# Kernel optimization log

Hardware: AMD Instinct MI355X
Metric: run time of the kernel (lower is better)

## Reference

```python
import jax, jax.numpy as jnp
import numpy as np

T, H, F, E, K, C = 8192, 1024, 2048, 16, 2, 1280  # tokens, hidden, ffn, experts, top_k, capacity


def setup_inputs() -> dict:
    key = jax.random.key(0)
    ks = jax.random.split(key, 6)
    return {
        "x": jax.random.normal(ks[0], (T, H), dtype=jnp.float32),
        "w_router": jax.random.normal(ks[1], (H, E), dtype=jnp.float32) * 0.02,
        "w1": jax.random.normal(ks[2], (E, H, F), dtype=jnp.float32) * 0.02,
        "b1": jnp.zeros((E, F), dtype=jnp.float32),
        "w2": jax.random.normal(ks[3], (E, F, H), dtype=jnp.float32) * 0.02,
        "b2": jnp.zeros((E, H), dtype=jnp.float32),
    }


def reference(x, w_router, w1, b1, w2, b2):
    # ---- Router: softmax + top-k (TopKRouter) ----
    logits = x @ w_router                                  # [T, E]
    probs = jax.nn.softmax(logits, axis=-1)
    topk_p, topk_idx = jax.lax.top_k(probs, K)             # [T, K]
    topk_p = topk_p / jnp.sum(topk_p, axis=-1, keepdims=True)

    # ---- Dispatch with capacity drop (token_permutation) ----
    flat_e = topk_idx.reshape(-1)                          # [T*K] expert id per assignment
    token_ids = jnp.repeat(jnp.arange(T), K)               # [T*K]
    oh = jax.nn.one_hot(flat_e, E, dtype=jnp.int32)        # [T*K, E]
    # position of each assignment within its expert's buffer (token order)
    pos = jnp.cumsum(oh, axis=0) - oh                      # [T*K, E]
    pos = jnp.take_along_axis(pos, flat_e[:, None], axis=1)[:, 0]  # [T*K]
    keep = pos < C
    safe_pos = jnp.where(keep, pos, C)                     # dropped tokens -> dummy slot C

    dispatched = jnp.zeros((E, C + 1, H), dtype=x.dtype)
    dispatched = dispatched.at[flat_e, safe_pos].add(x[token_ids])
    disp = dispatched[:, :C, :]                            # [E, C, H]

    # ---- Grouped expert MLP (SequentialMLP: fc1 -> gelu -> fc2) ----
    h = jax.nn.gelu(jnp.einsum("ech,ehf->ecf", disp, w1) + b1[:, None, :])
    y = jnp.einsum("ecf,efh->ech", h, w2) + b2[:, None, :]  # [E, C, H]

    # ---- Combine (token_unpermutation): gather + prob-weighted sum ----
    y_pad = jnp.pad(y, ((0, 0), (0, 1), (0, 0)))            # dummy slot returns garbage, masked below
    gathered = y_pad[flat_e, safe_pos]                      # [T*K, H]
    gathered = jnp.where(keep[:, None], gathered, 0.0)
    weighted = gathered * topk_p.reshape(-1)[:, None]
    out = jax.ops.segment_sum(weighted, token_ids, num_segments=T)  # [T, H]
    return out
```

## Files before the change

kernel.cpp:

```cpp
#include <hip/hip_runtime.h>
#include <cstdint>
#include <cstddef>

#define T_TOK 8192
#define HDIM  1024
#define FDIM  2048
#define NEXP  16
#define CAP   1280

typedef __bf16 bf16x8 __attribute__((ext_vector_type(8)));
typedef float  f32x4  __attribute__((ext_vector_type(4)));

__device__ inline void gld16(const void* g, void* l) {
  __builtin_amdgcn_global_load_lds(
      (__attribute__((address_space(1))) void*)g,
      (__attribute__((address_space(3))) void*)l, 16, 0, 0);
}

__global__ __launch_bounds__(256) void router_kernel(
    const float* __restrict__ x, const float* __restrict__ wr,
    int* __restrict__ eidx, float* __restrict__ eprob) {
  int t = blockIdx.x * 4 + (threadIdx.x >> 6);
  int lane = threadIdx.x & 63;
  float acc[NEXP];
#pragma unroll
  for (int e = 0; e < NEXP; ++e) acc[e] = 0.f;
  const float4* xp = (const float4*)(x + (size_t)t * HDIM + lane * 16);
#pragma unroll
  for (int q = 0; q < 4; ++q) {
    float4 xv = xp[q];
    float xa[4] = {xv.x, xv.y, xv.z, xv.w};
#pragma unroll
    for (int ii = 0; ii < 4; ++ii) {
      int h = lane * 16 + q * 4 + ii;
      const float4* wp = (const float4*)(wr + (size_t)h * NEXP);
      float w[NEXP];
      float4 w0 = wp[0], w1 = wp[1], w2 = wp[2], w3 = wp[3];
      w[0]=w0.x; w[1]=w0.y; w[2]=w0.z; w[3]=w0.w;
      w[4]=w1.x; w[5]=w1.y; w[6]=w1.z; w[7]=w1.w;
      w[8]=w2.x; w[9]=w2.y; w[10]=w2.z; w[11]=w2.w;
      w[12]=w3.x; w[13]=w3.y; w[14]=w3.z; w[15]=w3.w;
#pragma unroll
      for (int e = 0; e < NEXP; ++e) acc[e] += xa[ii] * w[e];
    }
  }
#pragma unroll
  for (int e = 0; e < NEXP; ++e) {
#pragma unroll
    for (int s = 32; s > 0; s >>= 1) acc[e] += __shfl_xor(acc[e], s);
  }
  if (lane == 0) {
    float l0 = -1e30f, l1 = -1e30f; int i0 = 0, i1 = 0;
#pragma unroll
    for (int e = 0; e < NEXP; ++e) {
      float v = acc[e];
      if (v > l0) { l1 = l0; i1 = i0; l0 = v; i0 = e; }
      else if (v > l1) { l1 = v; i1 = e; }
    }
    float p0 = 1.f / (1.f + __expf(l1 - l0));
    eidx[t * 2 + 0] = i0; eidx[t * 2 + 1] = i1;
    eprob[t * 2 + 0] = p0; eprob[t * 2 + 1] = 1.f - p0;
  }
}

__global__ __launch_bounds__(256) void pos_kernel(
    const int* __restrict__ eidx, const float* __restrict__ eprob,
    int* __restrict__ slot_token, float* __restrict__ slot_prob) {
  __shared__ int scan[256][NEXP];
  int tid = threadIdx.x;
  int cnt[NEXP];
#pragma unroll
  for (int e = 0; e < NEXP; ++e) cnt[e] = 0;
  int base_i = tid * 64;
  for (int i = 0; i < 64; ++i) cnt[eidx[base_i + i]]++;
#pragma unroll
  for (int e = 0; e < NEXP; ++e) scan[tid][e] = cnt[e];
  __syncthreads();
  if (tid < NEXP) {
    int run = 0;
    for (int i = 0; i < 256; ++i) { int v = scan[i][tid]; scan[i][tid] = run; run += v; }
  }
  __syncthreads();
  int basec[NEXP];
#pragma unroll
  for (int e = 0; e < NEXP; ++e) basec[e] = scan[tid][e];
  for (int i = 0; i < 64; ++i) {
    int fi = base_i + i;
    int e = eidx[fi];
    int p = basec[e]++;
    if (p < CAP) {
      slot_token[e * CAP + p] = fi >> 1;
      slot_prob[e * CAP + p] = eprob[fi];
    }
  }
}

__global__ __launch_bounds__(256) void scatter_kernel(
    const float* __restrict__ x, const int* __restrict__ slot_token,
    __bf16* __restrict__ disp) {
  int s = blockIdx.x * 4 + (threadIdx.x >> 6);
  int lane = threadIdx.x & 63;
  int tok = slot_token[s];
  __bf16 vals[16] __attribute__((aligned(16)));
  if (tok >= 0) {
    const float4* xp = (const float4*)(x + (size_t)tok * HDIM + lane * 16);
#pragma unroll
    for (int q = 0; q < 4; ++q) {
      float4 v = xp[q];
      vals[q * 4 + 0] = (__bf16)v.x; vals[q * 4 + 1] = (__bf16)v.y;
      vals[q * 4 + 2] = (__bf16)v.z; vals[q * 4 + 3] = (__bf16)v.w;
    }
  } else {
#pragma unroll
    for (int q = 0; q < 16; ++q) vals[q] = (__bf16)0.f;
  }
  uint4* dst = (uint4*)(disp + (size_t)s * HDIM + lane * 16);
  dst[0] = ((uint4*)vals)[0];
  dst[1] = ((uint4*)vals)[1];
}

__global__ __launch_bounds__(256) void transpose_cast_kernel(
    const float* __restrict__ src, __bf16* __restrict__ dst, int R, int Cc) {
  int e = blockIdx.z;
  src += (size_t)e * R * Cc;
  dst += (size_t)e * R * Cc;
  __shared__ float tile[64][65];
  int gy = blockIdx.y * 64;
  int gx = blockIdx.x * 64;
  int tid = threadIdx.x;
  int r = tid >> 4;
  int c4 = (tid & 15) * 4;
#pragma unroll
  for (int rr = 0; rr < 4; ++rr) {
    float4 v = *(const float4*)(src + (size_t)(gy + r + rr * 16) * Cc + gx + c4);
    tile[r + rr * 16][c4 + 0] = v.x;
    tile[r + rr * 16][c4 + 1] = v.y;
    tile[r + rr * 16][c4 + 2] = v.z;
    tile[r + rr * 16][c4 + 3] = v.w;
  }
  __syncthreads();
  int r2 = tid >> 2;
  int cb = (tid & 3) * 16;
  __bf16 o[16] __attribute__((aligned(16)));
#pragma unroll
  for (int i = 0; i < 16; ++i) o[i] = (__bf16)tile[cb + i][r2];
  uint4* dp = (uint4*)(dst + (size_t)(gx + r2) * R + gy + cb);
  dp[0] = ((uint4*)o)[0];
  dp[1] = ((uint4*)o)[1];
}

template <int EPI>
__global__ __launch_bounds__(256) void moe_gemm_kernel(
    const __bf16* __restrict__ A, const __bf16* __restrict__ Bt,
    const float* __restrict__ bias, __bf16* __restrict__ Hout,
    const int* __restrict__ slot_token, const float* __restrict__ slot_prob,
    float* __restrict__ out, int M, int N, int Kd) {
  const int e = blockIdx.z;
  const int m0 = blockIdx.y * 128, n0 = blockIdx.x * 128;
  const __bf16* Ae = A + (size_t)e * M * Kd;
  const __bf16* Be = Bt + (size_t)e * N * Kd;
  __shared__ __bf16 ldsA[128 * 64];
  __shared__ __bf16 ldsB[128 * 64];
  const int tid = threadIdx.x, wave = tid >> 6, lane = tid & 63;
  const int quad = lane >> 4, l15 = lane & 15;
  const int wm = (wave >> 1) * 64, wn = (wave & 1) * 64;
  f32x4 acc[4][4] = {};
  const int Kb = Kd * 2;
  const int ktiles = Kd >> 6;
  for (int kt = 0; kt < ktiles; ++kt) {
    __syncthreads();
#pragma unroll
    for (int rr = 0; rr < 4; ++rr) {
      int bofs = wave * 4096 + rr * 1024;
      int lofs = bofs + lane * 16;
      int row = lofs >> 7;
      int colb = lofs & 127;
      gld16((const char*)Ae + (size_t)(m0 + row) * Kb + kt * 128 + colb,
            (char*)ldsA + bofs);
      gld16((const char*)Be + (size_t)(n0 + row) * Kb + kt * 128 + colb,
            (char*)ldsB + bofs);
    }
    __syncthreads();
#pragma unroll
    for (int kk = 0; kk < 64; kk += 32) {
      bf16x8 av[4], bv[4];
#pragma unroll
      for (int i = 0; i < 4; ++i)
        av[i] = *(const bf16x8*)&ldsA[(wm + i * 16 + l15) * 64 + kk + quad * 8];
#pragma unroll
      for (int j = 0; j < 4; ++j)
        bv[j] = *(const bf16x8*)&ldsB[(wn + j * 16 + l15) * 64 + kk + quad * 8];
#pragma unroll
      for (int i = 0; i < 4; ++i)
#pragma unroll
        for (int j = 0; j < 4; ++j)
          acc[i][j] = __builtin_amdgcn_mfma_f32_16x16x32_bf16(av[i], bv[j], acc[i][j], 0, 0, 0);
    }
  }
  if (EPI == 1) {
    __bf16* He = Hout + (size_t)e * M * N;
#pragma unroll
    for (int i = 0; i < 4; ++i) {
#pragma unroll
      for (int r = 0; r < 4; ++r) {
        int m = m0 + wm + i * 16 + quad * 4 + r;
#pragma unroll
        for (int j = 0; j < 4; ++j) {
          int n = n0 + wn + j * 16 + l15;
          float v = acc[i][j][r] + bias[(size_t)e * N + n];
          float u = 0.7978845608028654f * (v + 0.044715f * v * v * v);
          float ex = __expf(-2.f * fabsf(u));
          float th = (1.f - ex) / (1.f + ex);
          th = copysignf(th, u);
          He[(size_t)m * N + n] = (__bf16)(0.5f * v * (1.f + th));
        }
      }
    }
  } else {
    const int* st = slot_token + e * CAP;
    const float* sp = slot_prob + e * CAP;
#pragma unroll
    for (int i = 0; i < 4; ++i) {
#pragma unroll
      for (int r = 0; r < 4; ++r) {
        int m = m0 + wm + i * 16 + quad * 4 + r;
        int tok = st[m];
        if (tok >= 0) {
          float p = sp[m];
#pragma unroll
          for (int j = 0; j < 4; ++j) {
            int n = n0 + wn + j * 16 + l15;
            float v = acc[i][j][r] + bias[(size_t)e * N + n];
            atomicAdd(out + (size_t)tok * HDIM + n, p * v);
          }
        }
      }
    }
  }
}

extern "C" void kernel_launch(void* const* d_in, const int* in_sizes, int n_in,
                              void* d_out, int out_size, void* d_ws, size_t ws_size,
                              hipStream_t stream) {
  const float* x  = (const float*)d_in[0];
  const float* wr = (const float*)d_in[1];
  const float* w1 = (const float*)d_in[2];
  const float* b1 = (const float*)d_in[3];
  const float* w2 = (const float*)d_in[4];
  const float* b2 = (const float*)d_in[5];
  float* out = (float*)d_out;

  char* ws = (char*)d_ws;
  size_t off = 0;
  __bf16* w1t = (__bf16*)(ws + off); off += (size_t)NEXP * FDIM * HDIM * 2;
  __bf16* w2t = (__bf16*)(ws + off); off += (size_t)NEXP * HDIM * FDIM * 2;
  __bf16* disp = (__bf16*)(ws + off); off += (size_t)NEXP * CAP * HDIM * 2;
  __bf16* hbuf = (__bf16*)(ws + off); off += (size_t)NEXP * CAP * FDIM * 2;
  int*   slot_token = (int*)(ws + off);  off += (size_t)NEXP * CAP * 4;
  float* slot_prob  = (float*)(ws + off); off += (size_t)NEXP * CAP * 4;
  int*   eidx  = (int*)(ws + off);  off += (size_t)T_TOK * 2 * 4;
  float* eprob = (float*)(ws + off); off += (size_t)T_TOK * 2 * 4;
  if (ws_size < off) return;

  hipMemsetAsync(slot_token, 0xFF, (size_t)NEXP * CAP * 4, stream);
  hipMemsetAsync(d_out, 0, (size_t)T_TOK * HDIM * 4, stream);

  transpose_cast_kernel<<<dim3(FDIM / 64, HDIM / 64, NEXP), 256, 0, stream>>>(w1, w1t, HDIM, FDIM);
  transpose_cast_kernel<<<dim3(HDIM / 64, FDIM / 64, NEXP), 256, 0, stream>>>(w2, w2t, FDIM, HDIM);

  router_kernel<<<T_TOK / 4, 256, 0, stream>>>(x, wr, eidx, eprob);
  pos_kernel<<<1, 256, 0, stream>>>(eidx, eprob, slot_token, slot_prob);
  scatter_kernel<<<NEXP * CAP / 4, 256, 0, stream>>>(x, slot_token, disp);

  moe_gemm_kernel<1><<<dim3(FDIM / 128, CAP / 128, NEXP), 256, 0, stream>>>(
      disp, w1t, b1, hbuf, nullptr, nullptr, nullptr, CAP, FDIM, HDIM);
  moe_gemm_kernel<2><<<dim3(HDIM / 128, CAP / 128, NEXP), 256, 0, stream>>>(
      hbuf, w2t, b2, nullptr, slot_token, slot_prob, out, CAP, HDIM, FDIM);
}
```

Before: 888.0 us.

## Double-buffer MoE GEMM LDS tiles with XOR swizzle and vectorize pos counting

The grouped GEMM now keeps two LDS buffers, so the global-to-LDS load of the next K tile is issued before the MFMA work on the current one, with a single waitcnt+barrier per iteration. The global source columns are XOR-swizzled by row so the LDS reads for MFMA operands avoid bank conflicts. The pos kernel's expert-count loop also reads eidx as int4. LDS use doubles to 64KB per block, which may lower occupancy. Correctness of the single-barrier scheme depends on the vmcnt wait covering the LDS-direct loads.

```diff
diff --git a/kernel.cpp b/kernel.cpp
--- a/kernel.cpp
+++ b/kernel.cpp
@@ -72,7 +72,11 @@
 #pragma unroll
   for (int e = 0; e < NEXP; ++e) cnt[e] = 0;
   int base_i = tid * 64;
-  for (int i = 0; i < 64; ++i) cnt[eidx[base_i + i]]++;
+  const int4* ep = (const int4*)(eidx + base_i);
+  for (int i = 0; i < 16; ++i) {
+    int4 v = ep[i];
+    cnt[v.x]++; cnt[v.y]++; cnt[v.z]++; cnt[v.w]++;
+  }
 #pragma unroll
   for (int e = 0; e < NEXP; ++e) scan[tid][e] = cnt[e];
   __syncthreads();
@@ -159,37 +163,61 @@
   const int m0 = blockIdx.y * 128, n0 = blockIdx.x * 128;
   const __bf16* Ae = A + (size_t)e * M * Kd;
   const __bf16* Be = Bt + (size_t)e * N * Kd;
-  __shared__ __bf16 ldsA[128 * 64];
-  __shared__ __bf16 ldsB[128 * 64];
+  __shared__ __bf16 lds[2 * 2 * 8192];
   const int tid = threadIdx.x, wave = tid >> 6, lane = tid & 63;
   const int quad = lane >> 4, l15 = lane & 15;
   const int wm = (wave >> 1) * 64, wn = (wave & 1) * 64;
   f32x4 acc[4][4] = {};
   const int Kb = Kd * 2;
   const int ktiles = Kd >> 6;
+
+  const int bofs0 = wave * 4096;
+  int srow[4], sgcol[4];
+#pragma unroll
+  for (int rr = 0; rr < 4; ++rr) {
+    int lofs = bofs0 + rr * 1024 + lane * 16;
+    int row = lofs >> 7;
+    int chunk = (lofs >> 4) & 7;
+    srow[rr] = row;
+    sgcol[rr] = (chunk ^ (row & 7)) * 16;
+  }
+
+  auto stage = [&](int kt, int b) {
+    char* dstA = (char*)lds + b * 32768;
+    char* dstB = dstA + 16384;
+#pragma unroll
+    for (int rr = 0; rr < 4; ++rr) {
+      int bofs = bofs0 + rr * 1024;
+      gld16((const char*)Ae + (size_t)(m0 + srow[rr]) * Kb + kt * 128 + sgcol[rr],
+            dstA + bofs);
+      gld16((const char*)Be + (size_t)(n0 + srow[rr]) * Kb + kt * 128 + sgcol[rr],
+            dstB + bofs);
+    }
+  };
+
+  stage(0, 0);
   for (int kt = 0; kt < ktiles; ++kt) {
-    __syncthreads();
-#pragma unroll
-    for (int rr = 0; rr < 4; ++rr) {
-      int bofs = wave * 4096 + rr * 1024;
-      int lofs = bofs + lane * 16;
-      int row = lofs >> 7;
-      int colb = lofs & 127;
-      gld16((const char*)Ae + (size_t)(m0 + row) * Kb + kt * 128 + colb,
-            (char*)ldsA + bofs);
-      gld16((const char*)Be + (size_t)(n0 + row) * Kb + kt * 128 + colb,
-            (char*)ldsB + bofs);
-    }
-    __syncthreads();
+    const int b = kt & 1;
+    __builtin_amdgcn_s_waitcnt(0x0f70);
+    __builtin_amdgcn_s_barrier();
+    if (kt + 1 < ktiles) stage(kt + 1, b ^ 1);
+    const __bf16* La = lds + b * 16384;
+    const __bf16* Lb = La + 8192;
 #pragma unroll
     for (int kk = 0; kk < 64; kk += 32) {
       bf16x8 av[4], bv[4];
 #pragma unroll
-      for (int i = 0; i < 4; ++i)
-        av[i] = *(const bf16x8*)&ldsA[(wm + i * 16 + l15) * 64 + kk + quad * 8];
-#pragma unroll
-      for (int j = 0; j < 4; ++j)
-        bv[j] = *(const bf16x8*)&ldsB[(wn + j * 16 + l15) * 64 + kk + quad * 8];
+      for (int i = 0; i < 4; ++i) {
+        int r = wm + i * 16 + l15;
+        int c = (kk >> 3) + quad;
+        av[i] = *(const bf16x8*)&La[r * 64 + ((c ^ (r & 7)) << 3)];
+      }
+#pragma unroll
+      for (int j = 0; j < 4; ++j) {
+        int r = wn + j * 16 + l15;
+        int c = (kk >> 3) + quad;
+        bv[j] = *(const bf16x8*)&Lb[r * 64 + ((c ^ (r & 7)) << 3)];
+      }
 #pragma unroll
       for (int i = 0; i < 4; ++i)
 #pragma unroll
```

After: 798.2 us. 1.11x faster.
